# Kernel optimization log

Measured on AMD Instinct MI355X. Metric: run time of the kernel, lower is better.

Reference implementation:

```python
import jax, jax.numpy as jnp
import numpy as np

B = 16384
NUM_ITEMS = 1_000_000
NUM_CATS = 1001  # num_categories + 1
USER_DIM = 64
ITEM_DIM = 64
CAT_DIM = 32  # item_embedding_dim // 2
DIM1 = 10000
DIM2 = 10000
DEEP_IN = USER_DIM + ITEM_DIM + CAT_DIM + 2 + 2  # 164
HID = [128, 64, 32]
BN_EPS = 1e-5


def setup_inputs() -> dict:
    key = jax.random.key(0)
    ks = jax.random.split(key, 24)
    inp = {
        'user_embeddings': jax.random.normal(ks[0], (B, USER_DIM), jnp.float32),
        'price_features': jax.random.normal(ks[1], (B, 2), jnp.float32),
        'temporal_features': jax.random.normal(ks[2], (B, 2), jnp.float32),
        'item_emb': jax.random.normal(ks[3], (NUM_ITEMS, ITEM_DIM), jnp.float32) * 0.02,
        'cat_emb': jax.random.normal(ks[4], (NUM_CATS, CAT_DIM), jnp.float32) * 0.02,
        'wide_emb1': jax.random.normal(ks[5], (DIM1, 1), jnp.float32) * 0.02,
        'wide_emb2': jax.random.normal(ks[6], (DIM2, 1), jnp.float32) * 0.02,
        'cross_W': jax.random.normal(ks[7], (DIM1 * DIM2,), jnp.float32) * 0.001,
        'item_ids': jax.random.randint(ks[8], (B,), 0, NUM_ITEMS),
        'category_ids': jax.random.randint(ks[9], (B,), 0, NUM_CATS),
        'wf1': jax.random.randint(ks[10], (B,), 0, DIM1),
        'wf2': jax.random.randint(ks[11], (B,), 0, DIM2),
    }
    dims = [DEEP_IN] + HID + [1]
    for i in range(4):
        fan_in = dims[i]
        inp[f'W{i+1}'] = jax.random.normal(ks[12 + i], (dims[i], dims[i + 1]), jnp.float32) / np.sqrt(fan_in)
        inp[f'b{i+1}'] = jnp.zeros((dims[i + 1],), jnp.float32)
    for i in range(3):  # batch-norm affine params (eval mode, running stats = 0/1)
        inp[f'g{i+1}'] = jnp.ones((HID[i],), jnp.float32)
        inp[f'be{i+1}'] = jnp.zeros((HID[i],), jnp.float32)
    return inp


def _bn(x, g, b):
    # eval-mode BatchNorm1d with running_mean=0, running_var=1
    return x * (g / jnp.sqrt(1.0 + BN_EPS)) + b


def reference(user_embeddings, price_features, temporal_features, item_emb, cat_emb,
              wide_emb1, wide_emb2, cross_W, W1, b1, W2, b2, W3, b3, W4, b4,
              g1, be1, g2, be2, g3, be3, item_ids, category_ids, wf1, wf2):
    # deep component
    x = jnp.concatenate([user_embeddings, item_emb[item_ids], cat_emb[category_ids],
                         price_features, temporal_features], axis=-1)  # [B, 164]
    x = jax.nn.relu(_bn(x @ W1 + b1, g1, be1))
    x = jax.nn.relu(_bn(x @ W2 + b2, g2, be2))
    x = jax.nn.relu(_bn(x @ W3 + b3, g3, be3))
    deep_out = x @ W4 + b4  # [B, 1]
    # wide component: per-feature 1-d embeddings + cross term.
    # one_hot(f1) outer one_hot(f2) flattened then dotted with cross_W is exactly
    # a gather at flat index f1*DIM2 + f2 (same math, no [B, DIM1*DIM2] intermediate).
    wide_out = wide_emb1[wf1] + wide_emb2[wf2]  # [B, 1]
    flat_idx = wf1 * DIM2 + wf2
    wide_out = wide_out + cross_W[flat_idx][:, None]
    return wide_out + deep_out
```

## Files before the change

kernel.cpp:

```cpp
#include <hip/hip_runtime.h>

#define NROWS     64
#define NTHREADS  1024
#define DEEP_IN   164
#define NCHUNK    41
#define XS_STRIDE 192
#define H1        128
#define H2        64
#define H3        32
#define DIM2_C    10000

#define XS_OFF  0
#define H1_OFF  (NROWS * XS_STRIDE)
#define H2_OFF  (H1_OFF + NROWS * H1)
#define H3_OFF  (H2_OFF + NROWS * H2)
#define WD_OFF  (H3_OFF + NROWS * H3)
#define ARENA_F (WD_OFF + NROWS)

__global__ __launch_bounds__(NTHREADS) void wad_fused(
    const float* __restrict__ user, const float* __restrict__ price,
    const float* __restrict__ temporal, const float* __restrict__ item_emb,
    const float* __restrict__ cat_emb, const float* __restrict__ we1,
    const float* __restrict__ we2, const float* __restrict__ crossW,
    const int* __restrict__ item_ids, const int* __restrict__ cat_ids,
    const int* __restrict__ wf1, const int* __restrict__ wf2,
    const float* __restrict__ W1, const float* __restrict__ b1,
    const float* __restrict__ W2, const float* __restrict__ b2,
    const float* __restrict__ W3, const float* __restrict__ b3,
    const float* __restrict__ W4, const float* __restrict__ b4,
    const float* __restrict__ g1, const float* __restrict__ be1,
    const float* __restrict__ g2, const float* __restrict__ be2,
    const float* __restrict__ g3, const float* __restrict__ be3,
    float* __restrict__ out)
{
    __shared__ float arena[ARENA_F];
    float* xs    = arena + XS_OFF;
    float* h1s   = arena + H1_OFF;
    float* h2s   = arena + H2_OFF;
    float* h3s   = arena + H3_OFF;
    float* wideS = arena + WD_OFF;

    const int tid  = threadIdx.x;
    const int lane = tid & 63;
    const int wave = tid >> 6;
    const int lx   = lane & 7;
    const int r0   = blockIdx.x * NROWS;

    const float bn_rs = rsqrtf(1.0f + 1e-5f);

    for (int idx = tid; idx < NROWS * NCHUNK; idx += NTHREADS) {
        int r  = idx / NCHUNK;
        int k4 = idx - r * NCHUNK;
        int R  = r0 + r;
        float4 v;
        if (k4 < 16)      v = *(const float4*)(user + R * 64 + k4 * 4);
        else if (k4 < 32) v = *(const float4*)(item_emb + item_ids[R] * 64 + (k4 - 16) * 4);
        else if (k4 < 40) v = *(const float4*)(cat_emb + cat_ids[R] * 32 + (k4 - 32) * 4);
        else {
            float2 p = *(const float2*)(price + R * 2);
            float2 t = *(const float2*)(temporal + R * 2);
            v = make_float4(p.x, p.y, t.x, t.y);
        }
        int kcs = k4 ^ (r & 7);
        *(float4*)(xs + r * XS_STRIDE + kcs * 4) = v;
    }
    if (tid < NROWS) {
        int R = r0 + tid;
        int f1 = wf1[R], f2 = wf2[R];
        wideS[tid] = we1[f1] + we2[f2] + crossW[f1 * DIM2_C + f2];
    }
    __syncthreads();

    {
        const int c0 = __builtin_amdgcn_readfirstlane(wave * 8);
        float acc[8];
#pragma unroll
        for (int n = 0; n < 8; ++n) acc[n] = 0.0f;
        const float* xrow = xs + lane * XS_STRIDE;
        for (int kq = 0; kq < NCHUNK; ++kq) {
            float4 a = *(const float4*)(xrow + (kq ^ lx) * 4);
            const float* wbase = W1 + kq * 4 * H1 + c0;
#pragma unroll
            for (int kk = 0; kk < 4; ++kk) {
                float av = ((const float*)&a)[kk];
#pragma unroll
                for (int n = 0; n < 8; ++n) acc[n] += av * wbase[kk * H1 + n];
            }
        }
#pragma unroll
        for (int n = 0; n < 8; n += 4) {
            float4 o;
#pragma unroll
            for (int e = 0; e < 4; ++e) {
                int c = c0 + n + e;
                float z = (acc[n + e] + b1[c]) * (g1[c] * bn_rs) + be1[c];
                ((float*)&o)[e] = fmaxf(z, 0.0f);
            }
            int kc  = (c0 + n) >> 2;
            int kcs = kc ^ lx;
            *(float4*)(h1s + lane * H1 + kcs * 4) = o;
        }
    }
    __syncthreads();

    {
        const int c02 = __builtin_amdgcn_readfirstlane(wave * 4);
        float acc2[4];
#pragma unroll
        for (int n = 0; n < 4; ++n) acc2[n] = 0.0f;
        for (int kq = 0; kq < H1 / 4; ++kq) {
            float4 a = *(const float4*)(h1s + lane * H1 + (kq ^ lx) * 4);
            const float* wbase = W2 + kq * 4 * H2 + c02;
#pragma unroll
            for (int kk = 0; kk < 4; ++kk) {
                float av = ((const float*)&a)[kk];
#pragma unroll
                for (int n = 0; n < 4; ++n) acc2[n] += av * wbase[kk * H2 + n];
            }
        }
        float4 o;
#pragma unroll
        for (int e = 0; e < 4; ++e) {
            int c = c02 + e;
            float z = (acc2[e] + b2[c]) * (g2[c] * bn_rs) + be2[c];
            ((float*)&o)[e] = fmaxf(z, 0.0f);
        }
        int kcs = wave ^ lx;
        *(float4*)(h2s + lane * H2 + kcs * 4) = o;
    }
    __syncthreads();

    {
        const int c03 = __builtin_amdgcn_readfirstlane(wave * 2);
        float acc3[2];
        acc3[0] = 0.0f; acc3[1] = 0.0f;
        for (int kq = 0; kq < H2 / 4; ++kq) {
            float4 a = *(const float4*)(h2s + lane * H2 + (kq ^ lx) * 4);
            const float* wbase = W3 + kq * 4 * H3 + c03;
#pragma unroll
            for (int kk = 0; kk < 4; ++kk) {
                float av = ((const float*)&a)[kk];
                acc3[0] += av * wbase[kk * H3];
                acc3[1] += av * wbase[kk * H3 + 1];
            }
        }
        float2 o;
        {
            int c = c03;
            float z0 = (acc3[0] + b3[c]) * (g3[c] * bn_rs) + be3[c];
            float z1 = (acc3[1] + b3[c + 1]) * (g3[c + 1] * bn_rs) + be3[c + 1];
            o.x = fmaxf(z0, 0.0f);
            o.y = fmaxf(z1, 0.0f);
        }
        int ps = wave ^ (lane & 15);
        *(float2*)(h3s + lane * H3 + ps * 2) = o;
    }
    __syncthreads();

    if (tid < NROWS) {
        int j = tid;
        float s = b4[0];
#pragma unroll
        for (int w = 0; w < 16; ++w) {
            int ps = w ^ (j & 15);
            float2 h = *(const float2*)(h3s + j * H3 + ps * 2);
            s += h.x * W4[2 * w] + h.y * W4[2 * w + 1];
        }
        out[r0 + j] = s + wideS[j];
    }
}

extern "C" void kernel_launch(void* const* d_in, const int* in_sizes, int n_in,
                              void* d_out, int out_size, void* d_ws, size_t ws_size,
                              hipStream_t stream) {
    const float* user     = (const float*)d_in[0];
    const float* price    = (const float*)d_in[1];
    const float* temporal = (const float*)d_in[2];
    const float* item_emb = (const float*)d_in[3];
    const float* cat_emb  = (const float*)d_in[4];
    const float* we1      = (const float*)d_in[5];
    const float* we2      = (const float*)d_in[6];
    const float* crossW   = (const float*)d_in[7];
    const int*   item_ids = (const int*)d_in[8];
    const int*   cat_ids  = (const int*)d_in[9];
    const int*   wf1      = (const int*)d_in[10];
    const int*   wf2      = (const int*)d_in[11];
    const float* W1 = (const float*)d_in[12];
    const float* b1 = (const float*)d_in[13];
    const float* W2 = (const float*)d_in[14];
    const float* b2 = (const float*)d_in[15];
    const float* W3 = (const float*)d_in[16];
    const float* b3 = (const float*)d_in[17];
    const float* W4 = (const float*)d_in[18];
    const float* b4 = (const float*)d_in[19];
    const float* g1  = (const float*)d_in[20];
    const float* be1 = (const float*)d_in[21];
    const float* g2  = (const float*)d_in[22];
    const float* be2 = (const float*)d_in[23];
    const float* g3  = (const float*)d_in[24];
    const float* be3 = (const float*)d_in[25];
    float* out = (float*)d_out;

    const int nblocks = 16384 / NROWS;
    wad_fused<<<nblocks, NTHREADS, 0, stream>>>(
        user, price, temporal, item_emb, cat_emb, we1, we2, crossW,
        item_ids, cat_ids, wf1, wf2,
        W1, b1, W2, b2, W3, b3, W4, b4,
        g1, be1, g2, be2, g3, be3, out);
}
```

Measured before the change: 616.1 us.

## Halve rows per block and split each wave across two column groups

Blocks now process 32 rows with 512 threads, and each wave covers 32 rows times two column groups (half-wave split) instead of 64 rows times one group. Twice as many blocks are launched, which is meant to improve occupancy and latency hiding. Weight loads are vectorised to float4/float2. In exchange, weight addresses are no longer wave-uniform, so they may turn from scalar loads into per-lane vector loads.

```diff
diff --git a/kernel.cpp b/kernel.cpp
--- a/kernel.cpp
+++ b/kernel.cpp
@@ -1,7 +1,7 @@
 #include <hip/hip_runtime.h>
 
-#define NROWS     64
-#define NTHREADS  1024
+#define NROWS     32
+#define NTHREADS  512
 #define DEEP_IN   164
 #define NCHUNK    41
 #define XS_STRIDE 192
@@ -43,7 +43,9 @@
     const int tid  = threadIdx.x;
     const int lane = tid & 63;
     const int wave = tid >> 6;
-    const int lx   = lane & 7;
+    const int row  = lane & 31;
+    const int half = lane >> 5;
+    const int rx   = row & 7;
     const int r0   = blockIdx.x * NROWS;
 
     const float bn_rs = rsqrtf(1.0f + 1e-5f);
@@ -72,19 +74,24 @@
     __syncthreads();
 
     {
-        const int c0 = __builtin_amdgcn_readfirstlane(wave * 8);
+        const int c0 = wave * 16 + half * 8;
         float acc[8];
 #pragma unroll
         for (int n = 0; n < 8; ++n) acc[n] = 0.0f;
-        const float* xrow = xs + lane * XS_STRIDE;
+        const float* xrow = xs + row * XS_STRIDE;
         for (int kq = 0; kq < NCHUNK; ++kq) {
-            float4 a = *(const float4*)(xrow + (kq ^ lx) * 4);
+            float4 a = *(const float4*)(xrow + (kq ^ rx) * 4);
             const float* wbase = W1 + kq * 4 * H1 + c0;
 #pragma unroll
             for (int kk = 0; kk < 4; ++kk) {
-                float av = ((const float*)&a)[kk];
-#pragma unroll
-                for (int n = 0; n < 8; ++n) acc[n] += av * wbase[kk * H1 + n];
+                float  av = ((const float*)&a)[kk];
+                float4 w0 = *(const float4*)(wbase + kk * H1);
+                float4 w1 = *(const float4*)(wbase + kk * H1 + 4);
+#pragma unroll
+                for (int e = 0; e < 4; ++e) {
+                    acc[e]     += av * ((const float*)&w0)[e];
+                    acc[4 + e] += av * ((const float*)&w1)[e];
+                }
             }
         }
 #pragma unroll
@@ -97,25 +104,26 @@
                 ((float*)&o)[e] = fmaxf(z, 0.0f);
             }
             int kc  = (c0 + n) >> 2;
-            int kcs = kc ^ lx;
-            *(float4*)(h1s + lane * H1 + kcs * 4) = o;
+            int kcs = kc ^ rx;
+            *(float4*)(h1s + row * H1 + kcs * 4) = o;
         }
     }
     __syncthreads();
 
     {
-        const int c02 = __builtin_amdgcn_readfirstlane(wave * 4);
+        const int c02 = wave * 8 + half * 4;
         float acc2[4];
 #pragma unroll
         for (int n = 0; n < 4; ++n) acc2[n] = 0.0f;
         for (int kq = 0; kq < H1 / 4; ++kq) {
-            float4 a = *(const float4*)(h1s + lane * H1 + (kq ^ lx) * 4);
+            float4 a = *(const float4*)(h1s + row * H1 + (kq ^ rx) * 4);
             const float* wbase = W2 + kq * 4 * H2 + c02;
 #pragma unroll
             for (int kk = 0; kk < 4; ++kk) {
-                float av = ((const float*)&a)[kk];
-#pragma unroll
-                for (int n = 0; n < 4; ++n) acc2[n] += av * wbase[kk * H2 + n];
+                float  av = ((const float*)&a)[kk];
+                float4 w  = *(const float4*)(wbase + kk * H2);
+#pragma unroll
+                for (int n = 0; n < 4; ++n) acc2[n] += av * ((const float*)&w)[n];
             }
         }
         float4 o;
@@ -125,23 +133,25 @@
             float z = (acc2[e] + b2[c]) * (g2[c] * bn_rs) + be2[c];
             ((float*)&o)[e] = fmaxf(z, 0.0f);
         }
-        int kcs = wave ^ lx;
-        *(float4*)(h2s + lane * H2 + kcs * 4) = o;
+        int kc  = c02 >> 2;
+        int kcs = kc ^ rx;
+        *(float4*)(h2s + row * H2 + kcs * 4) = o;
     }
     __syncthreads();
 
     {
-        const int c03 = __builtin_amdgcn_readfirstlane(wave * 2);
+        const int c03 = wave * 4 + half * 2;
         float acc3[2];
         acc3[0] = 0.0f; acc3[1] = 0.0f;
         for (int kq = 0; kq < H2 / 4; ++kq) {
-            float4 a = *(const float4*)(h2s + lane * H2 + (kq ^ lx) * 4);
+            float4 a = *(const float4*)(h2s + row * H2 + (kq ^ rx) * 4);
             const float* wbase = W3 + kq * 4 * H3 + c03;
 #pragma unroll
             for (int kk = 0; kk < 4; ++kk) {
-                float av = ((const float*)&a)[kk];
-                acc3[0] += av * wbase[kk * H3];
-                acc3[1] += av * wbase[kk * H3 + 1];
+                float  av = ((const float*)&a)[kk];
+                float2 w  = *(const float2*)(wbase + kk * H3);
+                acc3[0] += av * w.x;
+                acc3[1] += av * w.y;
             }
         }
         float2 o;
@@ -152,8 +162,9 @@
             o.x = fmaxf(z0, 0.0f);
             o.y = fmaxf(z1, 0.0f);
         }
-        int ps = wave ^ (lane & 15);
-        *(float2*)(h3s + lane * H3 + ps * 2) = o;
+        int p  = c03 >> 1;
+        int ps = p ^ (row & 15);
+        *(float2*)(h3s + row * H3 + ps * 2) = o;
     }
     __syncthreads();
 
```

After: 632.9 us. 2.7% more time.
